# Optimization experiments

Measured on AMD Instinct MI355X. Metric: run time of the kernel, lower is better.

Reference implementation:

```python
import jax, jax.numpy as jnp
import numpy as np

N_NODES = 20000
IN_DIM = 256
HID = 128
N_CLASSES = 64
N_EDGES = 320000
EPS_BN = 1e-5


def setup_inputs() -> dict:
    key = jax.random.key(0)
    ks = jax.random.split(key, 24)
    s = 0.1
    inp = {}
    inp['x'] = jax.random.normal(ks[0], (N_NODES, IN_DIM), dtype=jnp.float32)
    inp['edge_index'] = jax.random.randint(ks[1], (2, N_EDGES), 0, N_NODES, dtype=jnp.int32)
    # GATConv 1: in=IN_DIM, out=HID per head, heads=4, concat=False
    inp['W1'] = s * jax.random.normal(ks[2], (IN_DIM, 4 * HID), dtype=jnp.float32)
    inp['a_src1'] = s * jax.random.normal(ks[3], (4, HID), dtype=jnp.float32)
    inp['a_dst1'] = s * jax.random.normal(ks[4], (4, HID), dtype=jnp.float32)
    inp['b1'] = jnp.zeros((HID,), jnp.float32)
    # GATConv 2: in=HID, out=HID per head, heads=4, concat=False
    inp['W2'] = s * jax.random.normal(ks[5], (HID, 4 * HID), dtype=jnp.float32)
    inp['a_src2'] = s * jax.random.normal(ks[6], (4, HID), dtype=jnp.float32)
    inp['a_dst2'] = s * jax.random.normal(ks[7], (4, HID), dtype=jnp.float32)
    inp['b2'] = jnp.zeros((HID,), jnp.float32)
    # GATConv 3: heads=1, concat=True (default)
    inp['W3'] = s * jax.random.normal(ks[8], (HID, HID), dtype=jnp.float32)
    inp['a_src3'] = s * jax.random.normal(ks[9], (1, HID), dtype=jnp.float32)
    inp['a_dst3'] = s * jax.random.normal(ks[10], (1, HID), dtype=jnp.float32)
    inp['b3'] = jnp.zeros((HID,), jnp.float32)
    # BatchNorm (eval-mode running stats)
    for i, k in zip((1, 2), (ks[11], ks[12])):
        inp[f'bn{i}_g'] = jnp.ones((HID,), jnp.float32)
        inp[f'bn{i}_b'] = jnp.zeros((HID,), jnp.float32)
        inp[f'bn{i}_m'] = 0.01 * jax.random.normal(k, (HID,), dtype=jnp.float32)
        inp[f'bn{i}_v'] = jnp.ones((HID,), jnp.float32)
    # classifier MLP
    inp['l1_w'] = s * jax.random.normal(ks[13], (HID, HID), dtype=jnp.float32)
    inp['l1_b'] = jnp.zeros((HID,), jnp.float32)
    inp['l2_w'] = s * jax.random.normal(ks[14], (HID, HID // 2), dtype=jnp.float32)
    inp['l2_b'] = jnp.zeros((HID // 2,), jnp.float32)
    inp['l3_w'] = s * jax.random.normal(ks[15], (HID // 2, N_CLASSES), dtype=jnp.float32)
    inp['l3_b'] = jnp.zeros((N_CLASSES,), jnp.float32)
    return inp


def _gat(x, src, dst, W, a_src, a_dst, b, heads, out_ch, concat):
    """PyG GATConv (with self-loops already appended to src/dst)."""
    n = x.shape[0]
    h = (x @ W).reshape(n, heads, out_ch)            # [N,H,C]
    alpha_s = jnp.sum(h * a_src[None], axis=-1)       # [N,H]
    alpha_d = jnp.sum(h * a_dst[None], axis=-1)       # [N,H]
    e = jax.nn.leaky_relu(alpha_s[src] + alpha_d[dst], 0.2)  # [E,H]
    # segment softmax over incoming edges of each destination node
    m = jax.ops.segment_max(e, dst, num_segments=n)
    m = jnp.where(jnp.isfinite(m), m, 0.0)
    ex = jnp.exp(e - m[dst])
    den = jax.ops.segment_sum(ex, dst, num_segments=n)
    alpha = ex / (den[dst] + 1e-16)                   # [E,H]
    msg = h[src] * alpha[:, :, None]                  # [E,H,C]
    out = jax.ops.segment_sum(msg, dst, num_segments=n)  # [N,H,C]
    out = out.reshape(n, heads * out_ch) if concat else out.mean(axis=1)
    return out + b


def _bn_eval(x, g, b, m, v):
    return g * (x - m) * jax.lax.rsqrt(v + EPS_BN) + b


def reference(x, edge_index, W1, a_src1, a_dst1, b1, W2, a_src2, a_dst2, b2,
              W3, a_src3, a_dst3, b3, bn1_g, bn1_b, bn1_m, bn1_v,
              bn2_g, bn2_b, bn2_m, bn2_v, l1_w, l1_b, l2_w, l2_b, l3_w, l3_b):
    n = x.shape[0]
    loops = jnp.arange(n, dtype=edge_index.dtype)
    src = jnp.concatenate([edge_index[0], loops])
    dst = jnp.concatenate([edge_index[1], loops])

    h = _gat(x, src, dst, W1, a_src1, a_dst1, b1, 4, HID, False)
    h = jax.nn.relu(_bn_eval(h, bn1_g, bn1_b, bn1_m, bn1_v))
    h = _gat(h, src, dst, W2, a_src2, a_dst2, b2, 4, HID, False)
    h = jax.nn.relu(_bn_eval(h, bn2_g, bn2_b, bn2_m, bn2_v))
    h = _gat(h, src, dst, W3, a_src3, a_dst3, b3, 1, HID, True)

    h = jax.nn.relu(h @ l1_w + l1_b)
    h = jax.nn.relu(h @ l2_w + l2_b)
    return jax.nn.sigmoid(h @ l3_w + l3_b)  # [N, num_labels]
```

## Files before the change

### kernel.cpp

```cpp
#include <hip/hip_runtime.h>
#include <cstdint>
#include <cstddef>

#define NN 20000

typedef __bf16 bf16_t;
typedef __bf16 bf16x8 __attribute__((ext_vector_type(8)));
typedef float f32x4 __attribute__((ext_vector_type(4)));

#define AS1 __attribute__((address_space(1)))
#define AS3 __attribute__((address_space(3)))

__device__ __forceinline__ float lrelu(float x) { return x >= 0.f ? x : 0.2f * x; }
__device__ __forceinline__ float bflo(uint32_t u) { return __uint_as_float(u << 16); }
__device__ __forceinline__ float bfhi(uint32_t u) { return __uint_as_float(u & 0xffff0000u); }

__device__ __forceinline__ uint32_t pack2bf(float a, float b) {
  bf16_t x = (bf16_t)a, y = (bf16_t)b;
  uint16_t ux = __builtin_bit_cast(uint16_t, x);
  uint16_t uy = __builtin_bit_cast(uint16_t, y);
  return (uint32_t)ux | ((uint32_t)uy << 16);
}


__global__ __launch_bounds__(1024) void scan_kernel(const int* __restrict__ cnt,
                                                    int* __restrict__ row_ptr,
                                                    int* __restrict__ cursor, int n) {
  __shared__ int wsum[16];
  const int t = threadIdx.x;
  const int lane = t & 63, w = t >> 6;
  int carry = 0;
  for (int base = 0; base < n; base += 1024) {
    int i = base + t;
    int v = (i < n) ? cnt[i] : 0;
    int x = v;
#pragma unroll
    for (int d = 1; d < 64; d <<= 1) {
      int y = __shfl_up(x, d);
      if (lane >= d) x += y;
    }
    if (lane == 63) wsum[w] = x;
    __syncthreads();
    if (t < 16) {
      int s = wsum[t];
#pragma unroll
      for (int d = 1; d < 16; d <<= 1) {
        int y = __shfl_up(s, d);
        if (t >= d) s += y;
      }
      wsum[t] = s;
    }
    __syncthreads();
    int blocksum = wsum[15];
    int wprefix = (w == 0) ? 0 : wsum[w - 1];
    int excl = carry + wprefix + (x - v);
    if (i < n) { row_ptr[i] = excl; cursor[i] = excl; }
    carry += blocksum;
    __syncthreads();
  }
  if (t == 0) row_ptr[n] = carry;
}


struct WDesc { const float* W; bf16_t* Bt; int K; int Cw; int H; float scale; int b0; };
struct WPack { WDesc d[4]; };

struct Prep1Args {
  WPack wp;
  const float *W1, *as1, *ad1, *W2, *as2, *ad2, *W3, *as3, *ad3;
  float *P1, *P2, *P3;
  const float *W3m, *L1w, *b3v, *l1b;
  bf16_t* M3t; float* bm;
  const int* ei; int E, N, EB;
  int* cnt;
};

__global__ __launch_bounds__(256) void prep1(Prep1Args a) {
  __shared__ float tile[32][33];
  const int b = blockIdx.x;
  const int t = threadIdx.x;

  if (b < 204) {
    int i = 3;
#pragma unroll
    for (int k = 2; k >= 0; --k)
      if (b < a.wp.d[k + 1].b0) i = k;
    const WDesc de = a.wp.d[i];
    const int bi = b - de.b0;
    const int ktiles = de.K / 32;
    const int kt = bi % ktiles, rt = bi / ktiles;
    const int gc = rt * 32;
    const int h = gc / de.Cw, c0 = gc % de.Cw;
    const int tx = t & 31, ty = t >> 5;
#pragma unroll
    for (int r = 0; r < 32; r += 8)
      tile[ty + r][tx] = de.W[(size_t)(kt * 32 + ty + r) * (de.H * de.Cw) + h * de.Cw + c0 + tx];
    __syncthreads();
#pragma unroll
    for (int r = 0; r < 32; r += 8)
      de.Bt[(size_t)(c0 + ty + r) * (de.H * de.K) + h * de.K + kt * 32 + tx] =
          (bf16_t)(de.scale * tile[tx][ty + r]);
  } else if (b < 716) {
    const int kk = b - 204;
    const float *W, *asrc, *adst;
    float* P;
    int K, H, k;
    if (kk < 256)      { W = a.W1; asrc = a.as1; adst = a.ad1; P = a.P1; K = 256; H = 4; k = kk; }
    else if (kk < 384) { W = a.W2; asrc = a.as2; adst = a.ad2; P = a.P2; K = 128; H = 4; k = kk - 256; }
    else               { W = a.W3; asrc = a.as3; adst = a.ad3; P = a.P3; K = 128; H = 1; k = kk - 384; }
    for (int j = 0; j < 2 * H; ++j) {
      const int h = (j < H) ? j : j - H;
      const float* av = (j < H) ? asrc : adst;
      float pv = 0.f;
      if (t < 128) pv = W[(size_t)k * (H * 128) + h * 128 + t] * av[h * 128 + t];
#pragma unroll
      for (int d = 1; d < 64; d <<= 1) pv += __shfl_xor(pv, d);
      if (t == 0 || t == 64) tile[0][t >> 6] = pv;
      __syncthreads();
      if (t == 0) P[j * K + k] = tile[0][0] + tile[0][1];
      __syncthreads();
    }
  } else if (b < 780) {
    const int idx = (b - 716) * 256 + t;
    const int k = idx >> 7, c = idx & 127;
    float s = 0.f;
    for (int m = 0; m < 128; ++m) s += a.W3m[k * 128 + m] * a.L1w[m * 128 + c];
    a.M3t[c * 128 + k] = (bf16_t)s;
    if (k == 0) {
      float tt = a.l1b[c];
      for (int m = 0; m < 128; ++m) tt += a.b3v[m] * a.L1w[m * 128 + c];
      a.bm[c] = tt;
    }
  } else {
    const int i = (b - 780) * 256 + t;
    if (i < a.E + a.N) {
      int dst = (i < a.E) ? a.ei[a.E + i] : (i - a.E);
      atomicAdd(&a.cnt[dst], 1);
    }
  }
}


__global__ __launch_bounds__(256) void scatter_cast(const int* __restrict__ ei, int E, int N,
                                                    int EB, int* __restrict__ cursor,
                                                    int* __restrict__ col,
                                                    const float* __restrict__ x,
                                                    const float* __restrict__ P1,
                                                    bf16_t* __restrict__ xb,
                                                    float* __restrict__ asadA) {
  const int b = blockIdx.x, t = threadIdx.x;
  if (b < EB) {
    const int i = b * 256 + t;
    if (i < E + N) {
      int src, dst;
      if (i < E) { src = ei[i]; dst = ei[E + i]; }
      else       { src = i - E; dst = src; }
      int slot = atomicAdd(&cursor[dst], 1);
      col[slot] = src;
    }
  } else {
    const int wv = t >> 6, lane = t & 63;
    const int n = (b - EB) * 4 + wv;
    const float4 v = *(const float4*)&x[(size_t)n * 256 + lane * 4];
    uint2 ov;
    ov.x = pack2bf(v.x, v.y);
    ov.y = pack2bf(v.z, v.w);
    *(uint2*)&xb[(size_t)n * 256 + lane * 4] = ov;
    float s[8];
#pragma unroll
    for (int j = 0; j < 8; ++j) {
      const float4 pj = *(const float4*)&P1[j * 256 + lane * 4];
      s[j] = v.x * pj.x + v.y * pj.y + v.z * pj.z + v.w * pj.w;
    }
#pragma unroll
    for (int j = 0; j < 8; ++j)
#pragma unroll
      for (int d = 1; d < 64; d <<= 1) s[j] += __shfl_xor(s[j], d);
    if (lane == 0) {
#pragma unroll
      for (int j = 0; j < 8; ++j) asadA[(size_t)n * 8 + j] = s[j];
    }
  }
}


template <int TN, int ACT, typename OUT_T>
__global__ __launch_bounds__(256) void gemm_mfma(const bf16_t* __restrict__ A,
                                                 const bf16_t* __restrict__ Bt,
                                                 const float* __restrict__ bias,
                                                 const float* __restrict__ bng,
                                                 const float* __restrict__ bnb,
                                                 const float* __restrict__ bnm,
                                                 const float* __restrict__ bnv,
                                                 OUT_T* __restrict__ C,
                                                 int M, int N, int K) {
  constexpr int TM = 128, BK = 64;
  constexpr int MT = (TN == 128) ? 4 : 2;
  constexpr int NRB = (TN * BK * 2) / 4096;
  __shared__ __align__(16) bf16_t As[TM * BK];
  __shared__ __align__(16) bf16_t Bs[TN * BK];

  const int t = threadIdx.x;
  const int wave = t >> 6, lane = t & 63;
  const int ln15 = lane & 15, quad = lane >> 4;
  const int bm = blockIdx.x * TM;
  const int bn = blockIdx.y * TN;
  const int wm = (TN == 128) ? (wave >> 1) * 64 : wave * 32;
  const int wn = (TN == 128) ? (wave & 1) * 64 : 0;
  const int rowLimA = M - 1 - bm;
  const size_t strideAB = (size_t)K * 2;

  f32x4 acc[MT][4];
#pragma unroll
  for (int mi = 0; mi < MT; ++mi)
#pragma unroll
    for (int ni = 0; ni < 4; ++ni) acc[mi][ni] = (f32x4){0.f, 0.f, 0.f, 0.f};

  const char* gA = (const char*)(A + (size_t)bm * K);
  const char* gB = (const char*)(Bt + (size_t)bn * K);

  for (int k0 = 0; k0 < K; k0 += BK) {
#pragma unroll
    for (int r = 0; r < 4; ++r) {
      int base = (wave * 4 + r) * 1024;
      int flat = base + lane * 16;
      int row = flat >> 7;
      int grow = row < rowLimA ? row : rowLimA;
      const char* gp = gA + (size_t)grow * strideAB + (size_t)(k0 * 2) + (flat & 127);
      __builtin_amdgcn_global_load_lds((const AS1 void*)gp,
                                       (AS3 void*)((char*)As + base), 16, 0, 0);
    }
#pragma unroll
    for (int r = 0; r < NRB; ++r) {
      int base = (wave * NRB + r) * 1024;
      int flat = base + lane * 16;
      int row = flat >> 7;
      const char* gp = gB + (size_t)row * strideAB + (size_t)(k0 * 2) + (flat & 127);
      __builtin_amdgcn_global_load_lds((const AS1 void*)gp,
                                       (AS3 void*)((char*)Bs + base), 16, 0, 0);
    }
    __syncthreads();
#pragma unroll
    for (int kk = 0; kk < BK; kk += 32) {
      bf16x8 af[MT], bfr[4];
#pragma unroll
      for (int mi = 0; mi < MT; ++mi)
        af[mi] = *(const bf16x8*)&As[(wm + mi * 16 + ln15) * BK + kk + quad * 8];
#pragma unroll
      for (int ni = 0; ni < 4; ++ni)
        bfr[ni] = *(const bf16x8*)&Bs[(wn + ni * 16 + ln15) * BK + kk + quad * 8];
#pragma unroll
      for (int mi = 0; mi < MT; ++mi)
#pragma unroll
        for (int ni = 0; ni < 4; ++ni)
          acc[mi][ni] = __builtin_amdgcn_mfma_f32_16x16x32_bf16(af[mi], bfr[ni], acc[mi][ni], 0, 0, 0);
    }
    __syncthreads();
  }

#pragma unroll
  for (int mi = 0; mi < MT; ++mi) {
    int r0 = bm + wm + mi * 16 + quad * 4;
#pragma unroll
    for (int ni = 0; ni < 4; ++ni) {
      int c = bn + wn + ni * 16 + ln15;
      float bv = bias ? bias[c] : 0.f;
      float sc = 1.f, sh = 0.f;
      if (ACT == 3) {
        sc = bng[c] * rsqrtf(bnv[c] + 1e-5f);
        sh = bnb[c] - bnm[c] * sc;
      }
#pragma unroll
      for (int reg = 0; reg < 4; ++reg) {
        int r = r0 + reg;
        if (r < M) {
          float v = acc[mi][ni][reg] + bv;
          if (ACT == 1) v = fmaxf(v, 0.f);
          else if (ACT == 3) v = fmaxf(v * sc + sh, 0.f);
          C[(size_t)r * N + c] = (OUT_T)v;
        }
      }
    }
  }
}


template <int K, int H>
__global__ __launch_bounds__(256) void alpha_gemm(const bf16_t* __restrict__ f,
                                                  const float* __restrict__ P,
                                                  float* __restrict__ asad) {
  constexpr int J = 2 * H;
  constexpr int KC = K / 64;
  const int wv = threadIdx.x >> 6, lane = threadIdx.x & 63;
  const int n = blockIdx.x * 4 + wv;
  float v[KC];
  if (KC == 4) {
    uint2 pv = *(const uint2*)&f[(size_t)n * K + lane * 4];
    v[0] = bflo(pv.x); v[1] = bfhi(pv.x); v[2] = bflo(pv.y); v[3] = bfhi(pv.y);
  } else {
    uint32_t pv = *(const uint32_t*)&f[(size_t)n * K + lane * 2];
    v[0] = bflo(pv); v[1] = bfhi(pv);
  }
  float s[J];
#pragma unroll
  for (int j = 0; j < J; ++j) {
    float acc = 0.f;
#pragma unroll
    for (int q = 0; q < KC; ++q) acc += v[q] * P[j * K + lane * KC + q];
    s[j] = acc;
  }
#pragma unroll
  for (int j = 0; j < J; ++j)
#pragma unroll
    for (int d = 1; d < 64; d <<= 1) s[j] += __shfl_xor(s[j], d);
  if (lane == 0) {
#pragma unroll
    for (int j = 0; j < J; ++j) asad[(size_t)n * J + j] = s[j];
  }
}


template <int K>
__global__ __launch_bounds__(128) void gat_agg_in4(const bf16_t* __restrict__ f,
                                                   const float* __restrict__ asad,
                                                   const int* __restrict__ rp,
                                                   const int* __restrict__ cs,
                                                   bf16_t* __restrict__ agg) {
  constexpr int KC = K / 64;
  const int wv = threadIdx.x >> 6, lane = threadIdx.x & 63;
  const int n = blockIdx.x * 2 + wv;
  __shared__ int sb[2][64];
  __shared__ float4 wl[2][64];

  const int r0 = rp[n], r1 = rp[n + 1];
  const int deg = r1 - r0;
  const float4 adv = *(const float4*)&asad[(size_t)n * 8 + 4];
  const char* fb = (const char*)f;
  const size_t loff = (size_t)lane * (KC * 2);

  float acc[4][KC];
#pragma unroll
  for (int j = 0; j < 4; ++j)
#pragma unroll
    for (int q = 0; q < KC; ++q) acc[j][q] = 0.f;

  auto edge_fma = [&](const char* gp, float4 w4) {
    if (KC == 4) {
      uint2 b = *(const uint2*)gp;
      float v0 = bflo(b.x), v1 = bfhi(b.x), v2 = bflo(b.y), v3 = bfhi(b.y);
      acc[0][0] += w4.x * v0; acc[0][1] += w4.x * v1; acc[0][2] += w4.x * v2; acc[0][3] += w4.x * v3;
      acc[1][0] += w4.y * v0; acc[1][1] += w4.y * v1; acc[1][2] += w4.y * v2; acc[1][3] += w4.y * v3;
      acc[2][0] += w4.z * v0; acc[2][1] += w4.z * v1; acc[2][2] += w4.z * v2; acc[2][3] += w4.z * v3;
      acc[3][0] += w4.w * v0; acc[3][1] += w4.w * v1; acc[3][2] += w4.w * v2; acc[3][3] += w4.w * v3;
    } else {
      uint32_t b = *(const uint32_t*)gp;
      float v0 = bflo(b), v1 = bfhi(b);
      acc[0][0] += w4.x * v0; acc[0][1] += w4.x * v1;
      acc[1][0] += w4.y * v0; acc[1][1] += w4.y * v1;
      acc[2][0] += w4.z * v0; acc[2][1] += w4.z * v1;
      acc[3][0] += w4.w * v0; acc[3][1] += w4.w * v1;
    }
  };

  if (deg <= 64) {
    const bool valid = lane < deg;
    int s = 0;
    float e0 = -1e30f, e1 = -1e30f, e2 = -1e30f, e3 = -1e30f;
    if (valid) {
      s = cs[r0 + lane];
      const float4 av = *(const float4*)&asad[(size_t)s * 8];
      e0 = lrelu(av.x + adv.x); e1 = lrelu(av.y + adv.y);
      e2 = lrelu(av.z + adv.z); e3 = lrelu(av.w + adv.w);
    }
    float m0 = e0, m1 = e1, m2 = e2, m3 = e3;
#pragma unroll
    for (int d = 1; d < 64; d <<= 1) {
      m0 = fmaxf(m0, __shfl_xor(m0, d)); m1 = fmaxf(m1, __shfl_xor(m1, d));
      m2 = fmaxf(m2, __shfl_xor(m2, d)); m3 = fmaxf(m3, __shfl_xor(m3, d));
    }
    float x0 = valid ? __expf(e0 - m0) : 0.f;
    float x1 = valid ? __expf(e1 - m1) : 0.f;
    float x2 = valid ? __expf(e2 - m2) : 0.f;
    float x3 = valid ? __expf(e3 - m3) : 0.f;
    float d0 = x0, d1 = x1, d2 = x2, d3 = x3;
#pragma unroll
    for (int d = 1; d < 64; d <<= 1) {
      d0 += __shfl_xor(d0, d); d1 += __shfl_xor(d1, d);
      d2 += __shfl_xor(d2, d); d3 += __shfl_xor(d3, d);
    }
    if (valid) {
      sb[wv][lane] = s * (K * 2);
      wl[wv][lane] = make_float4(x0 / (d0 + 1e-16f), x1 / (d1 + 1e-16f),
                                 x2 / (d2 + 1e-16f), x3 / (d3 + 1e-16f));
    }
    __builtin_amdgcn_wave_barrier();

    int g = 0;
    for (; g + 8 <= deg; g += 8) {
      const char* p[8];
      float4 w[8];
#pragma unroll
      for (int k = 0; k < 8; ++k) { p[k] = fb + (size_t)sb[wv][g + k] + loff; w[k] = wl[wv][g + k]; }
      if (KC == 4) {
        uint2 b[8];
#pragma unroll
        for (int k = 0; k < 8; ++k) b[k] = *(const uint2*)p[k];
#pragma unroll
        for (int k = 0; k < 8; ++k) {
          float v0 = bflo(b[k].x), v1 = bfhi(b[k].x), v2 = bflo(b[k].y), v3 = bfhi(b[k].y);
          acc[0][0] += w[k].x * v0; acc[0][1] += w[k].x * v1; acc[0][2] += w[k].x * v2; acc[0][3] += w[k].x * v3;
          acc[1][0] += w[k].y * v0; acc[1][1] += w[k].y * v1; acc[1][2] += w[k].y * v2; acc[1][3] += w[k].y * v3;
          acc[2][0] += w[k].z * v0; acc[2][1] += w[k].z * v1; acc[2][2] += w[k].z * v2; acc[2][3] += w[k].z * v3;
          acc[3][0] += w[k].w * v0; acc[3][1] += w[k].w * v1; acc[3][2] += w[k].w * v2; acc[3][3] += w[k].w * v3;
        }
      } else {
        uint32_t b[8];
#pragma unroll
        for (int k = 0; k < 8; ++k) b[k] = *(const uint32_t*)p[k];
#pragma unroll
        for (int k = 0; k < 8; ++k) {
          float v0 = bflo(b[k]), v1 = bfhi(b[k]);
          acc[0][0] += w[k].x * v0; acc[0][1] += w[k].x * v1;
          acc[1][0] += w[k].y * v0; acc[1][1] += w[k].y * v1;
          acc[2][0] += w[k].z * v0; acc[2][1] += w[k].z * v1;
          acc[3][0] += w[k].w * v0; acc[3][1] += w[k].w * v1;
        }
      }
    }
    for (; g < deg; ++g)
      edge_fma(fb + (size_t)sb[wv][g] + loff, wl[wv][g]);
  } else {
    float m0 = -1e30f, m1 = -1e30f, m2 = -1e30f, m3 = -1e30f;
    for (int i = r0 + lane; i < r1; i += 64) {
      const float4 av = *(const float4*)&asad[(size_t)cs[i] * 8];
      m0 = fmaxf(m0, lrelu(av.x + adv.x)); m1 = fmaxf(m1, lrelu(av.y + adv.y));
      m2 = fmaxf(m2, lrelu(av.z + adv.z)); m3 = fmaxf(m3, lrelu(av.w + adv.w));
    }
#pragma unroll
    for (int d = 1; d < 64; d <<= 1) {
      m0 = fmaxf(m0, __shfl_xor(m0, d)); m1 = fmaxf(m1, __shfl_xor(m1, d));
      m2 = fmaxf(m2, __shfl_xor(m2, d)); m3 = fmaxf(m3, __shfl_xor(m3, d));
    }
    float d0 = 0.f, d1 = 0.f, d2 = 0.f, d3 = 0.f;
    for (int i = r0 + lane; i < r1; i += 64) {
      const float4 av = *(const float4*)&asad[(size_t)cs[i] * 8];
      d0 += __expf(lrelu(av.x + adv.x) - m0); d1 += __expf(lrelu(av.y + adv.y) - m1);
      d2 += __expf(lrelu(av.z + adv.z) - m2); d3 += __expf(lrelu(av.w + adv.w) - m3);
    }
#pragma unroll
    for (int d = 1; d < 64; d <<= 1) {
      d0 += __shfl_xor(d0, d); d1 += __shfl_xor(d1, d);
      d2 += __shfl_xor(d2, d); d3 += __shfl_xor(d3, d);
    }
    const float i0 = 1.f / (d0 + 1e-16f), i1 = 1.f / (d1 + 1e-16f);
    const float i2 = 1.f / (d2 + 1e-16f), i3 = 1.f / (d3 + 1e-16f);
    for (int base = r0; base < r1; base += 64) {
      const int ne = min(64, r1 - base);
      if (lane < ne) {
        const int s = cs[base + lane];
        const float4 av = *(const float4*)&asad[(size_t)s * 8];
        sb[wv][lane] = s * (K * 2);
        wl[wv][lane] = make_float4(__expf(lrelu(av.x + adv.x) - m0) * i0,
                                   __expf(lrelu(av.y + adv.y) - m1) * i1,
                                   __expf(lrelu(av.z + adv.z) - m2) * i2,
                                   __expf(lrelu(av.w + adv.w) - m3) * i3);
      }
      __builtin_amdgcn_wave_barrier();
      for (int g = 0; g < ne; ++g)
        edge_fma(fb + (size_t)sb[wv][g] + loff, wl[wv][g]);
      __builtin_amdgcn_wave_barrier();
    }
  }

#pragma unroll
  for (int j = 0; j < 4; ++j) {
    if (KC == 4) {
      uint2 ov;
      ov.x = pack2bf(acc[j][0], acc[j][1]);
      ov.y = pack2bf(acc[j][2], acc[j][3]);
      *(uint2*)&agg[(size_t)n * (4 * K) + j * K + lane * 4] = ov;
    } else {
      *(uint32_t*)&agg[(size_t)n * (4 * K) + j * K + lane * 2] = pack2bf(acc[j][0], acc[j][1]);
    }
  }
}


__global__ __launch_bounds__(128) void gat_agg_in1(const bf16_t* __restrict__ f,
                                                   const float* __restrict__ asad,
                                                   const int* __restrict__ rp,
                                                   const int* __restrict__ cs,
                                                   bf16_t* __restrict__ agg) {
  const int wv = threadIdx.x >> 6, lane = threadIdx.x & 63;
  const int n = blockIdx.x * 2 + wv;
  __shared__ int sb[2][64];
  __shared__ float wl[2][64];

  const int r0 = rp[n], r1 = rp[n + 1];
  const int deg = r1 - r0;
  const float adv = asad[(size_t)n * 2 + 1];
  const char* fb = (const char*)f;
  const size_t loff = (size_t)lane * 4;
  float a0 = 0.f, a1 = 0.f;

  auto fma2 = [&](uint32_t v, float w) { a0 += w * bflo(v); a1 += w * bfhi(v); };

  if (deg <= 64) {
    const bool valid = lane < deg;
    int s = 0;
    float e = -1e30f;
    if (valid) { s = cs[r0 + lane]; e = lrelu(asad[(size_t)s * 2] + adv); }
    float m = e;
#pragma unroll
    for (int d = 1; d < 64; d <<= 1) m = fmaxf(m, __shfl_xor(m, d));
    float x = valid ? __expf(e - m) : 0.f;
    float den = x;
#pragma unroll
    for (int d = 1; d < 64; d <<= 1) den += __shfl_xor(den, d);
    if (valid) { sb[wv][lane] = s * 256; wl[wv][lane] = x / (den + 1e-16f); }
    __builtin_amdgcn_wave_barrier();
    int g = 0;
    for (; g + 8 <= deg; g += 8) {
      uint32_t b[8];
      float w[8];
#pragma unroll
      for (int k = 0; k < 8; ++k) {
        b[k] = *(const uint32_t*)(fb + (size_t)sb[wv][g + k] + loff);
        w[k] = wl[wv][g + k];
      }
#pragma unroll
      for (int k = 0; k < 8; ++k) { a0 += w[k] * bflo(b[k]); a1 += w[k] * bfhi(b[k]); }
    }
    for (; g < deg; ++g)
      fma2(*(const uint32_t*)(fb + (size_t)sb[wv][g] + loff), wl[wv][g]);
  } else {
    float m = -1e30f;
    for (int i = r0 + lane; i < r1; i += 64) m = fmaxf(m, lrelu(asad[(size_t)cs[i] * 2] + adv));
#pragma unroll
    for (int d = 1; d < 64; d <<= 1) m = fmaxf(m, __shfl_xor(m, d));
    float den = 0.f;
    for (int i = r0 + lane; i < r1; i += 64) den += __expf(lrelu(asad[(size_t)cs[i] * 2] + adv) - m);
#pragma unroll
    for (int d = 1; d < 64; d <<= 1) den += __shfl_xor(den, d);
    const float dinv = 1.f / (den + 1e-16f);
    for (int base = r0; base < r1; base += 64) {
      const int ne = min(64, r1 - base);
      if (lane < ne) {
        const int s = cs[base + lane];
        sb[wv][lane] = s * 256;
        wl[wv][lane] = __expf(lrelu(asad[(size_t)s * 2] + adv) - m) * dinv;
      }
      __builtin_amdgcn_wave_barrier();
      for (int g = 0; g < ne; ++g)
        fma2(*(const uint32_t*)(fb + (size_t)sb[wv][g] + loff), wl[wv][g]);
      __builtin_amdgcn_wave_barrier();
    }
  }
  *(uint32_t*)&agg[(size_t)n * 128 + lane * 2] = pack2bf(a0, a1);
}


__global__ __launch_bounds__(256) void mlp_tail(const bf16_t* __restrict__ A,
                                                const bf16_t* __restrict__ M3t,
                                                const float* __restrict__ bm,
                                                const bf16_t* __restrict__ l2t,
                                                const float* __restrict__ l2b,
                                                const bf16_t* __restrict__ l3t,
                                                const float* __restrict__ l3b,
                                                float* __restrict__ out, int M) {
  __shared__ __align__(16) bf16_t As[128 * 128];
  __shared__ __align__(16) bf16_t Ws[128 * 128];
  const int t = threadIdx.x, wave = t >> 6, lane = t & 63;
  const int ln15 = lane & 15, quad = lane >> 4;
  const int bmr = blockIdx.x * 128;
  const int rowLim = M - 1 - bmr;

#pragma unroll
  for (int r = 0; r < 8; ++r) {
    int base = (wave * 8 + r) * 1024;
    int flat = base + lane * 16;
    int row = flat >> 8;
    int grow = row < rowLim ? row : rowLim;
    const char* gp = (const char*)A + (size_t)grow * 256 + (flat & 255);
    __builtin_amdgcn_global_load_lds((const AS1 void*)gp,
                                     (AS3 void*)((char*)As + base), 16, 0, 0);
  }
#pragma unroll
  for (int r = 0; r < 8; ++r) {
    int base = (wave * 8 + r) * 1024;
    __builtin_amdgcn_global_load_lds((const AS1 void*)((const char*)M3t + base + lane * 16),
                                     (AS3 void*)((char*)Ws + base), 16, 0, 0);
  }
  __syncthreads();

  const int wm = wave * 32;
  f32x4 a1[2][8];
#pragma unroll
  for (int mi = 0; mi < 2; ++mi)
#pragma unroll
    for (int ni = 0; ni < 8; ++ni) a1[mi][ni] = (f32x4){0.f, 0.f, 0.f, 0.f};
#pragma unroll
  for (int kk = 0; kk < 128; kk += 32) {
    bf16x8 af[2];
#pragma unroll
    for (int mi = 0; mi < 2; ++mi)
      af[mi] = *(const bf16x8*)&As[(wm + mi * 16 + ln15) * 128 + kk + quad * 8];
#pragma unroll
    for (int ni = 0; ni < 8; ++ni) {
      bf16x8 bf = *(const bf16x8*)&Ws[(ni * 16 + ln15) * 128 + kk + quad * 8];
#pragma unroll
      for (int mi = 0; mi < 2; ++mi)
        a1[mi][ni] = __builtin_amdgcn_mfma_f32_16x16x32_bf16(af[mi], bf, a1[mi][ni], 0, 0, 0);
    }
  }
  __syncthreads();

#pragma unroll
  for (int r = 0; r < 4; ++r) {
    int base = (wave * 4 + r) * 1024;
    __builtin_amdgcn_global_load_lds((const AS1 void*)((const char*)l2t + base + lane * 16),
                                     (AS3 void*)((char*)Ws + base), 16, 0, 0);
  }
#pragma unroll
  for (int r = 0; r < 2; ++r) {
    int base = (wave * 2 + r) * 1024;
    __builtin_amdgcn_global_load_lds((const AS1 void*)((const char*)l3t + base + lane * 16),
                                     (AS3 void*)((char*)Ws + 8192 * 2 + base), 16, 0, 0);
  }
#pragma unroll
  for (int mi = 0; mi < 2; ++mi) {
    int r0 = wm + mi * 16 + quad * 4;
#pragma unroll
    for (int ni = 0; ni < 8; ++ni) {
      int c = ni * 16 + ln15;
      float bv = bm[c];
#pragma unroll
      for (int reg = 0; reg < 4; ++reg)
        As[(r0 + reg) * 128 + c] = (bf16_t)fmaxf(a1[mi][ni][reg] + bv, 0.f);
    }
  }
  __syncthreads();

  f32x4 a2[2][4];
#pragma unroll
  for (int mi = 0; mi < 2; ++mi)
#pragma unroll
    for (int ni = 0; ni < 4; ++ni) a2[mi][ni] = (f32x4){0.f, 0.f, 0.f, 0.f};
#pragma unroll
  for (int kk = 0; kk < 128; kk += 32) {
    bf16x8 af[2];
#pragma unroll
    for (int mi = 0; mi < 2; ++mi)
      af[mi] = *(const bf16x8*)&As[(wm + mi * 16 + ln15) * 128 + kk + quad * 8];
#pragma unroll
    for (int ni = 0; ni < 4; ++ni) {
      bf16x8 bf = *(const bf16x8*)&Ws[(ni * 16 + ln15) * 128 + kk + quad * 8];
#pragma unroll
      for (int mi = 0; mi < 2; ++mi)
        a2[mi][ni] = __builtin_amdgcn_mfma_f32_16x16x32_bf16(af[mi], bf, a2[mi][ni], 0, 0, 0);
    }
  }
  __syncthreads();

#pragma unroll
  for (int mi = 0; mi < 2; ++mi) {
    int r0 = wm + mi * 16 + quad * 4;
#pragma unroll
    for (int ni = 0; ni < 4; ++ni) {
      int c = ni * 16 + ln15;
      float bv = l2b[c];
#pragma unroll
      for (int reg = 0; reg < 4; ++reg)
        As[(r0 + reg) * 64 + c] = (bf16_t)fmaxf(a2[mi][ni][reg] + bv, 0.f);
    }
  }
  __syncthreads();

  f32x4 a3[2][4];
#pragma unroll
  for (int mi = 0; mi < 2; ++mi)
#pragma unroll
    for (int ni = 0; ni < 4; ++ni) a3[mi][ni] = (f32x4){0.f, 0.f, 0.f, 0.f};
#pragma unroll
  for (int kk = 0; kk < 64; kk += 32) {
    bf16x8 af[2];
#pragma unroll
    for (int mi = 0; mi < 2; ++mi)
      af[mi] = *(const bf16x8*)&As[(wm + mi * 16 + ln15) * 64 + kk + quad * 8];
#pragma unroll
    for (int ni = 0; ni < 4; ++ni) {
      bf16x8 bf = *(const bf16x8*)&Ws[8192 + (ni * 16 + ln15) * 64 + kk + quad * 8];
#pragma unroll
      for (int mi = 0; mi < 2; ++mi)
        a3[mi][ni] = __builtin_amdgcn_mfma_f32_16x16x32_bf16(af[mi], bf, a3[mi][ni], 0, 0, 0);
    }
  }
#pragma unroll
  for (int mi = 0; mi < 2; ++mi) {
    int r0 = wm + mi * 16 + quad * 4;
#pragma unroll
    for (int ni = 0; ni < 4; ++ni) {
      int c = ni * 16 + ln15;
      float bv = l3b[c];
#pragma unroll
      for (int reg = 0; reg < 4; ++reg) {
        int r = bmr + r0 + reg;
        if (r < M) {
          float v = a3[mi][ni][reg] + bv;
          out[(size_t)r * 64 + c] = 1.f / (1.f + __expf(-v));
        }
      }
    }
  }
}


extern "C" void kernel_launch(void* const* d_in, const int* in_sizes, int n_in,
                              void* d_out, int out_size, void* d_ws, size_t ws_size,
                              hipStream_t stream) {
  const float* x      = (const float*)d_in[0];
  const int*   ei     = (const int*)d_in[1];
  const float* W1     = (const float*)d_in[2];
  const float* a_src1 = (const float*)d_in[3];
  const float* a_dst1 = (const float*)d_in[4];
  const float* b1     = (const float*)d_in[5];
  const float* W2     = (const float*)d_in[6];
  const float* a_src2 = (const float*)d_in[7];
  const float* a_dst2 = (const float*)d_in[8];
  const float* b2     = (const float*)d_in[9];
  const float* W3     = (const float*)d_in[10];
  const float* a_src3 = (const float*)d_in[11];
  const float* a_dst3 = (const float*)d_in[12];
  const float* b3     = (const float*)d_in[13];
  const float* bn1g = (const float*)d_in[14];
  const float* bn1b = (const float*)d_in[15];
  const float* bn1m = (const float*)d_in[16];
  const float* bn1v = (const float*)d_in[17];
  const float* bn2g = (const float*)d_in[18];
  const float* bn2b = (const float*)d_in[19];
  const float* bn2m = (const float*)d_in[20];
  const float* bn2v = (const float*)d_in[21];
  const float* l1w = (const float*)d_in[22];
  const float* l1b = (const float*)d_in[23];
  const float* l2w = (const float*)d_in[24];
  const float* l2b = (const float*)d_in[25];
  const float* l3w = (const float*)d_in[26];
  const float* l3b = (const float*)d_in[27];
  float* out = (float*)d_out;

  const int N = NN;
  const int E = in_sizes[1] / 2;
  const int ET = E + N;
  const int EB = (ET + 255) / 256;

  char* p = (char*)d_ws;
  auto carve = [&](size_t bytes) {
    char* q = p;
    p += (bytes + 255) & ~(size_t)255;
    return q;
  };
  bf16_t* xb    = (bf16_t*)carve((size_t)N * 256 * 2);
  bf16_t* aggb  = (bf16_t*)carve((size_t)N * 1024 * 2);
  bf16_t* f1b   = (bf16_t*)carve((size_t)N * 128 * 2);
  bf16_t* f2b   = (bf16_t*)carve((size_t)N * 128 * 2);
  float* asadA  = (float*)carve((size_t)N * 8 * 4);
  float* asadB  = (float*)carve((size_t)N * 8 * 4);
  float* asadC  = (float*)carve((size_t)N * 2 * 4);
  int* cnt      = (int*)carve((size_t)N * 4);
  int* cursor   = (int*)carve((size_t)N * 4);
  int* row_ptr  = (int*)carve((size_t)(N + 1) * 4);
  int* col      = (int*)carve((size_t)ET * 4);
  bf16_t* Ws1t  = (bf16_t*)carve((size_t)128 * 1024 * 2);
  bf16_t* Ws2t  = (bf16_t*)carve((size_t)128 * 512 * 2);
  bf16_t* M3t   = (bf16_t*)carve((size_t)128 * 128 * 2);
  bf16_t* l2t   = (bf16_t*)carve((size_t)64 * 128 * 2);
  bf16_t* l3t   = (bf16_t*)carve((size_t)64 * 64 * 2);
  float* P1     = (float*)carve((size_t)8 * 256 * 4);
  float* P2     = (float*)carve((size_t)8 * 128 * 4);
  float* P3     = (float*)carve((size_t)2 * 128 * 4);
  float* bm     = (float*)carve((size_t)128 * 4);
  (void)ws_size; (void)n_in; (void)out_size;

  hipMemsetAsync(cnt, 0, (size_t)N * 4, stream);

  Prep1Args pa;
  pa.wp.d[0] = {W1,  Ws1t, 256, 128, 4, 0.25f, 0};
  pa.wp.d[1] = {W2,  Ws2t, 128, 128, 4, 0.25f, 128};
  pa.wp.d[2] = {l2w, l2t,  128, 64,  1, 1.0f,  192};
  pa.wp.d[3] = {l3w, l3t,  64,  64,  1, 1.0f,  200};
  pa.W1 = W1; pa.as1 = a_src1; pa.ad1 = a_dst1;
  pa.W2 = W2; pa.as2 = a_src2; pa.ad2 = a_dst2;
  pa.W3 = W3; pa.as3 = a_src3; pa.ad3 = a_dst3;
  pa.P1 = P1; pa.P2 = P2; pa.P3 = P3;
  pa.W3m = W3; pa.L1w = l1w; pa.b3v = b3; pa.l1b = l1b;
  pa.M3t = M3t; pa.bm = bm;
  pa.ei = ei; pa.E = E; pa.N = N; pa.EB = EB;
  pa.cnt = cnt;
  prep1<<<780 + EB, 256, 0, stream>>>(pa);

  scan_kernel<<<1, 1024, 0, stream>>>(cnt, row_ptr, cursor, N);
  scatter_cast<<<EB + N / 4, 256, 0, stream>>>(ei, E, N, EB, cursor, col, x, P1, xb, asadA);

  const int gm = (N + 127) / 128;
  const int ab = N / 4;
  const int gb = N / 2;

  gat_agg_in4<256><<<gb, 128, 0, stream>>>(xb, asadA, row_ptr, col, aggb);
  gemm_mfma<64, 3, bf16_t><<<dim3(gm, 2), 256, 0, stream>>>(
      aggb, Ws1t, b1, bn1g, bn1b, bn1m, bn1v, f1b, N, 128, 1024);

  alpha_gemm<128, 4><<<ab, 256, 0, stream>>>(f1b, P2, asadB);
  gat_agg_in4<128><<<gb, 128, 0, stream>>>(f1b, asadB, row_ptr, col, aggb);
  gemm_mfma<64, 3, bf16_t><<<dim3(gm, 2), 256, 0, stream>>>(
      aggb, Ws2t, b2, bn2g, bn2b, bn2m, bn2v, f2b, N, 128, 512);

  alpha_gemm<128, 1><<<ab, 256, 0, stream>>>(f2b, P3, asadC);
  gat_agg_in1<<<gb, 128, 0, stream>>>(f2b, asadC, row_ptr, col, aggb);
  mlp_tail<<<gm, 256, 0, stream>>>(aggb, M3t, bm, l2t, l2b, l3t, l3b, out, N);
}
```

Measured before the change: 337.9 us.

## Fuse post-scan pipeline into one persistent cooperative kernel with grid syncs

Replaces the sequence of separate launches (scatter/cast, three gathers, two GEMMs, two alpha projections, MLP tail) with one cooperative persistent kernel. Stages are separated by grid-wide barriers, and blocks loop over tiles or node groups in grid-stride fashion. The fused MLP tail is split into three separate GEMM stages that round-trip through global memory, and the aggregation now packs four nodes per block instead of two. This removes launch gaps and tail effects, but adds grid.sync costs, lower occupancy for the gather stages, and extra global traffic in the MLP.

```diff
diff --git a/kernel.cpp b/kernel.cpp
--- a/kernel.cpp
+++ b/kernel.cpp
@@ -1,6 +1,9 @@
 #include <hip/hip_runtime.h>
+#include <hip/hip_cooperative_groups.h>
 #include <cstdint>
 #include <cstddef>
+
+namespace cg = cooperative_groups;
 
 #define NN 20000
 
@@ -141,35 +144,46 @@
 }
 
 
-__global__ __launch_bounds__(256) void scatter_cast(const int* __restrict__ ei, int E, int N,
-                                                    int EB, int* __restrict__ cursor,
-                                                    int* __restrict__ col,
-                                                    const float* __restrict__ x,
-                                                    const float* __restrict__ P1,
-                                                    bf16_t* __restrict__ xb,
-                                                    float* __restrict__ asadA) {
-  const int b = blockIdx.x, t = threadIdx.x;
-  if (b < EB) {
+struct MegaArgs {
+  const int* ei; int E, N, EB;
+  int* cursor; int* col;
+  const float* x; const float* P1;
+  bf16_t* xb; float* asadA;
+  bf16_t *aggb, *f1b, *f2b;
+  float *asadB, *asadC;
+  const int* rp;
+  const bf16_t *Ws1t, *Ws2t, *M3t, *l2t, *l3t;
+  const float *P2, *P3;
+  const float *b1, *bn1g, *bn1b, *bn1m, *bn1v;
+  const float *b2, *bn2g, *bn2b, *bn2m, *bn2v;
+  const float *bm, *l2b, *l3b;
+  float* out;
+};
+
+
+__device__ void scatter_cast_dev(const MegaArgs& a, int b) {
+  const int t = threadIdx.x;
+  if (b < a.EB) {
     const int i = b * 256 + t;
-    if (i < E + N) {
+    if (i < a.E + a.N) {
       int src, dst;
-      if (i < E) { src = ei[i]; dst = ei[E + i]; }
-      else       { src = i - E; dst = src; }
-      int slot = atomicAdd(&cursor[dst], 1);
-      col[slot] = src;
+      if (i < a.E) { src = a.ei[i]; dst = a.ei[a.E + i]; }
+      else         { src = i - a.E; dst = src; }
+      int slot = atomicAdd(&a.cursor[dst], 1);
+      a.col[slot] = src;
     }
   } else {
     const int wv = t >> 6, lane = t & 63;
-    const int n = (b - EB) * 4 + wv;
-    const float4 v = *(const float4*)&x[(size_t)n * 256 + lane * 4];
+    const int n = (b - a.EB) * 4 + wv;
+    const float4 v = *(const float4*)&a.x[(size_t)n * 256 + lane * 4];
     uint2 ov;
     ov.x = pack2bf(v.x, v.y);
     ov.y = pack2bf(v.z, v.w);
-    *(uint2*)&xb[(size_t)n * 256 + lane * 4] = ov;
+    *(uint2*)&a.xb[(size_t)n * 256 + lane * 4] = ov;
     float s[8];
 #pragma unroll
     for (int j = 0; j < 8; ++j) {
-      const float4 pj = *(const float4*)&P1[j * 256 + lane * 4];
+      const float4 pj = *(const float4*)&a.P1[j * 256 + lane * 4];
       s[j] = v.x * pj.x + v.y * pj.y + v.z * pj.z + v.w * pj.w;
     }
 #pragma unroll
@@ -178,540 +192,422 @@
       for (int d = 1; d < 64; d <<= 1) s[j] += __shfl_xor(s[j], d);
     if (lane == 0) {
 #pragma unroll
-      for (int j = 0; j < 8; ++j) asadA[(size_t)n * 8 + j] = s[j];
+      for (int j = 0; j < 8; ++j) a.asadA[(size_t)n * 8 + j] = s[j];
     }
   }
 }
 
-
-template <int TN, int ACT, typename OUT_T>
-__global__ __launch_bounds__(256) void gemm_mfma(const bf16_t* __restrict__ A,
-                                                 const bf16_t* __restrict__ Bt,
-                                                 const float* __restrict__ bias,
-                                                 const float* __restrict__ bng,
-                                                 const float* __restrict__ bnb,
-                                                 const float* __restrict__ bnm,
-                                                 const float* __restrict__ bnv,
-                                                 OUT_T* __restrict__ C,
-                                                 int M, int N, int K) {
-  constexpr int TM = 128, BK = 64;
-  constexpr int MT = (TN == 128) ? 4 : 2;
-  constexpr int NRB = (TN * BK * 2) / 4096;
-  __shared__ __align__(16) bf16_t As[TM * BK];
-  __shared__ __align__(16) bf16_t Bs[TN * BK];
-
+__device__ void gemm_dev(char* smem, const bf16_t* A, const bf16_t* Bt,
+                         const float* bias, const float* bng, const float* bnb,
+                         const float* bnm, const float* bnv, int act,
+                         bf16_t* Cb, float* Cf, int M, int N, int K) {
+  bf16_t* As = (bf16_t*)smem;
+  bf16_t* Bs = (bf16_t*)(smem + 16384);
   const int t = threadIdx.x;
   const int wave = t >> 6, lane = t & 63;
   const int ln15 = lane & 15, quad = lane >> 4;
-  const int bm = blockIdx.x * TM;
-  const int bn = blockIdx.y * TN;
-  const int wm = (TN == 128) ? (wave >> 1) * 64 : wave * 32;
-  const int wn = (TN == 128) ? (wave & 1) * 64 : 0;
-  const int rowLimA = M - 1 - bm;
+  const int gx = (M + 127) >> 7;
+  const int ntile = gx * (N >> 6);
   const size_t strideAB = (size_t)K * 2;
 
-  f32x4 acc[MT][4];
-#pragma unroll
-  for (int mi = 0; mi < MT; ++mi)
-#pragma unroll
-    for (int ni = 0; ni < 4; ++ni) acc[mi][ni] = (f32x4){0.f, 0.f, 0.f, 0.f};
-
-  const char* gA = (const char*)(A + (size_t)bm * K);
-  const char* gB = (const char*)(Bt + (size_t)bn * K);
-
-  for (int k0 = 0; k0 < K; k0 += BK) {
-#pragma unroll
-    for (int r = 0; r < 4; ++r) {
-      int base = (wave * 4 + r) * 1024;
-      int flat = base + lane * 16;
-      int row = flat >> 7;
-      int grow = row < rowLimA ? row : rowLimA;
-      const char* gp = gA + (size_t)grow * strideAB + (size_t)(k0 * 2) + (flat & 127);
-      __builtin_amdgcn_global_load_lds((const AS1 void*)gp,
-                                       (AS3 void*)((char*)As + base), 16, 0, 0);
-    }
-#pragma unroll
-    for (int r = 0; r < NRB; ++r) {
-      int base = (wave * NRB + r) * 1024;
-      int flat = base + lane * 16;
-      int row = flat >> 7;
-      const char* gp = gB + (size_t)row * strideAB + (size_t)(k0 * 2) + (flat & 127);
-      __builtin_amdgcn_global_load_lds((const AS1 void*)gp,
-                                       (AS3 void*)((char*)Bs + base), 16, 0, 0);
-    }
-    __syncthreads();
-#pragma unroll
-    for (int kk = 0; kk < BK; kk += 32) {
-      bf16x8 af[MT], bfr[4];
-#pragma unroll
-      for (int mi = 0; mi < MT; ++mi)
-        af[mi] = *(const bf16x8*)&As[(wm + mi * 16 + ln15) * BK + kk + quad * 8];
-#pragma unroll
-      for (int ni = 0; ni < 4; ++ni)
-        bfr[ni] = *(const bf16x8*)&Bs[(wn + ni * 16 + ln15) * BK + kk + quad * 8];
-#pragma unroll
-      for (int mi = 0; mi < MT; ++mi)
+  for (int tile = blockIdx.x; tile < ntile; tile += gridDim.x) {
+    const int bm = (tile % gx) * 128;
+    const int bn = (tile / gx) * 64;
+    const int wm = wave * 32;
+    const int rowLimA = M - 1 - bm;
+
+    f32x4 acc[2][4];
+#pragma unroll
+    for (int mi = 0; mi < 2; ++mi)
+#pragma unroll
+      for (int ni = 0; ni < 4; ++ni) acc[mi][ni] = (f32x4){0.f, 0.f, 0.f, 0.f};
+
+    const char* gA = (const char*)A + (size_t)bm * strideAB;
+    const char* gB = (const char*)Bt + (size_t)bn * strideAB;
+
+    for (int k0 = 0; k0 < K; k0 += 64) {
+#pragma unroll
+      for (int r = 0; r < 4; ++r) {
+        int base = (wave * 4 + r) * 1024;
+        int flat = base + lane * 16;
+        int row = flat >> 7;
+        int grow = row < rowLimA ? row : rowLimA;
+        const char* gp = gA + (size_t)grow * strideAB + (size_t)(k0 * 2) + (flat & 127);
+        __builtin_amdgcn_global_load_lds((const AS1 void*)gp,
+                                         (AS3 void*)((char*)As + base), 16, 0, 0);
+      }
+#pragma unroll
+      for (int r = 0; r < 2; ++r) {
+        int base = (wave * 2 + r) * 1024;
+        int flat = base + lane * 16;
+        int row = flat >> 7;
+        const char* gp = gB + (size_t)row * strideAB + (size_t)(k0 * 2) + (flat & 127);
+        __builtin_amdgcn_global_load_lds((const AS1 void*)gp,
+                                         (AS3 void*)((char*)Bs + base), 16, 0, 0);
+      }
+      __syncthreads();
+#pragma unroll
+      for (int kk = 0; kk < 64; kk += 32) {
+        bf16x8 af[2], bfr[4];
+#pragma unroll
+        for (int mi = 0; mi < 2; ++mi)
+          af[mi] = *(const bf16x8*)&As[(wm + mi * 16 + ln15) * 64 + kk + quad * 8];
 #pragma unroll
         for (int ni = 0; ni < 4; ++ni)
-          acc[mi][ni] = __builtin_amdgcn_mfma_f32_16x16x32_bf16(af[mi], bfr[ni], acc[mi][ni], 0, 0, 0);
-    }
-    __syncthreads();
+          bfr[ni] = *(const bf16x8*)&Bs[(ni * 16 + ln15) * 64 + kk + quad * 8];
+#pragma unroll
+        for (int mi = 0; mi < 2; ++mi)
+#pragma unroll
+          for (int ni = 0; ni < 4; ++ni)
+            acc[mi][ni] = __builtin_amdgcn_mfma_f32_16x16x32_bf16(af[mi], bfr[ni], acc[mi][ni], 0, 0, 0);
+      }
+      __syncthreads();
+    }
+
+#pragma unroll
+    for (int mi = 0; mi < 2; ++mi) {
+      int r0 = bm + wm + mi * 16 + quad * 4;
+#pragma unroll
+      for (int ni = 0; ni < 4; ++ni) {
+        int c = bn + ni * 16 + ln15;
+        float bv = bias[c];
+        float sc = 1.f, sh = 0.f;
+        if (act == 3) {
+          sc = bng[c] * rsqrtf(bnv[c] + 1e-5f);
+          sh = bnb[c] - bnm[c] * sc;
+        }
+#pragma unroll
+        for (int reg = 0; reg < 4; ++reg) {
+          int r = r0 + reg;
+          if (r < M) {
+            float v = acc[mi][ni][reg] + bv;
+            if (act == 1) v = fmaxf(v, 0.f);
+            else if (act == 2) v = 1.f / (1.f + __expf(-v));
+            else v = fmaxf(v * sc + sh, 0.f);
+            if (Cb) Cb[(size_t)r * N + c] = (bf16_t)v;
+            else    Cf[(size_t)r * N + c] = v;
+          }
+        }
+      }
+    }
   }
-
-#pragma unroll
-  for (int mi = 0; mi < MT; ++mi) {
-    int r0 = bm + wm + mi * 16 + quad * 4;
-#pragma unroll
-    for (int ni = 0; ni < 4; ++ni) {
-      int c = bn + wn + ni * 16 + ln15;
-      float bv = bias ? bias[c] : 0.f;
-      float sc = 1.f, sh = 0.f;
-      if (ACT == 3) {
-        sc = bng[c] * rsqrtf(bnv[c] + 1e-5f);
-        sh = bnb[c] - bnm[c] * sc;
-      }
-#pragma unroll
-      for (int reg = 0; reg < 4; ++reg) {
-        int r = r0 + reg;
-        if (r < M) {
-          float v = acc[mi][ni][reg] + bv;
-          if (ACT == 1) v = fmaxf(v, 0.f);
-          else if (ACT == 3) v = fmaxf(v * sc + sh, 0.f);
-          C[(size_t)r * N + c] = (OUT_T)v;
-        }
-      }
-    }
-  }
-}
-
+}
 
 template <int K, int H>
-__global__ __launch_bounds__(256) void alpha_gemm(const bf16_t* __restrict__ f,
-                                                  const float* __restrict__ P,
-                                                  float* __restrict__ asad) {
+__device__ void alpha_dev(const bf16_t* f, const float* P, float* asad, int N) {
   constexpr int J = 2 * H;
   constexpr int KC = K / 64;
   const int wv = threadIdx.x >> 6, lane = threadIdx.x & 63;
-  const int n = blockIdx.x * 4 + wv;
-  float v[KC];
-  if (KC == 4) {
-    uint2 pv = *(const uint2*)&f[(size_t)n * K + lane * 4];
-    v[0] = bflo(pv.x); v[1] = bfhi(pv.x); v[2] = bflo(pv.y); v[3] = bfhi(pv.y);
-  } else {
-    uint32_t pv = *(const uint32_t*)&f[(size_t)n * K + lane * 2];
-    v[0] = bflo(pv); v[1] = bfhi(pv);
+  for (int grp = blockIdx.x; grp < N / 4; grp += gridDim.x) {
+    const int n = grp * 4 + wv;
+    float v[KC];
+    if (KC == 4) {
+      uint2 pv = *(const uint2*)&f[(size_t)n * K + lane * 4];
+      v[0] = bflo(pv.x); v[1] = bfhi(pv.x); v[2] = bflo(pv.y); v[3] = bfhi(pv.y);
+    } else {
+      uint32_t pv = *(const uint32_t*)&f[(size_t)n * K + lane * 2];
+      v[0] = bflo(pv); v[1] = bfhi(pv);
+    }
+    float s[J];
+#pragma unroll
+    for (int j = 0; j < J; ++j) {
+      float acc = 0.f;
+#pragma unroll
+      for (int q = 0; q < KC; ++q) acc += v[q] * P[j * K + lane * KC + q];
+      s[j] = acc;
+    }
+#pragma unroll
+    for (int j = 0; j < J; ++j)
+#pragma unroll
+      for (int d = 1; d < 64; d <<= 1) s[j] += __shfl_xor(s[j], d);
+    if (lane == 0) {
+#pragma unroll
+      for (int j = 0; j < J; ++j) asad[(size_t)n * J + j] = s[j];
+    }
   }
-  float s[J];
-#pragma unroll
-  for (int j = 0; j < J; ++j) {
-    float acc = 0.f;
-#pragma unroll
-    for (int q = 0; q < KC; ++q) acc += v[q] * P[j * K + lane * KC + q];
-    s[j] = acc;
-  }
-#pragma unroll
-  for (int j = 0; j < J; ++j)
-#pragma unroll
-    for (int d = 1; d < 64; d <<= 1) s[j] += __shfl_xor(s[j], d);
-  if (lane == 0) {
-#pragma unroll
-    for (int j = 0; j < J; ++j) asad[(size_t)n * J + j] = s[j];
-  }
-}
-
+}
 
 template <int K>
-__global__ __launch_bounds__(128) void gat_agg_in4(const bf16_t* __restrict__ f,
-                                                   const float* __restrict__ asad,
-                                                   const int* __restrict__ rp,
-                                                   const int* __restrict__ cs,
-                                                   bf16_t* __restrict__ agg) {
+__device__ void gather4_dev(char* smem, const bf16_t* f, const float* asad,
+                            const int* rp, const int* cs, bf16_t* agg, int N) {
   constexpr int KC = K / 64;
+  int* sb = (int*)smem;
+  float4* wl = (float4*)(smem + 1024);
   const int wv = threadIdx.x >> 6, lane = threadIdx.x & 63;
-  const int n = blockIdx.x * 2 + wv;
-  __shared__ int sb[2][64];
-  __shared__ float4 wl[2][64];
-
-  const int r0 = rp[n], r1 = rp[n + 1];
-  const int deg = r1 - r0;
-  const float4 adv = *(const float4*)&asad[(size_t)n * 8 + 4];
   const char* fb = (const char*)f;
   const size_t loff = (size_t)lane * (KC * 2);
 
-  float acc[4][KC];
-#pragma unroll
-  for (int j = 0; j < 4; ++j)
-#pragma unroll
-    for (int q = 0; q < KC; ++q) acc[j][q] = 0.f;
-
-  auto edge_fma = [&](const char* gp, float4 w4) {
-    if (KC == 4) {
-      uint2 b = *(const uint2*)gp;
-      float v0 = bflo(b.x), v1 = bfhi(b.x), v2 = bflo(b.y), v3 = bfhi(b.y);
-      acc[0][0] += w4.x * v0; acc[0][1] += w4.x * v1; acc[0][2] += w4.x * v2; acc[0][3] += w4.x * v3;
-      acc[1][0] += w4.y * v0; acc[1][1] += w4.y * v1; acc[1][2] += w4.y * v2; acc[1][3] += w4.y * v3;
-      acc[2][0] += w4.z * v0; acc[2][1] += w4.z * v1; acc[2][2] += w4.z * v2; acc[2][3] += w4.z * v3;
-      acc[3][0] += w4.w * v0; acc[3][1] += w4.w * v1; acc[3][2] += w4.w * v2; acc[3][3] += w4.w * v3;
+  for (int grp = blockIdx.x; grp < N / 4; grp += gridDim.x) {
+    const int n = grp * 4 + wv;
+    const int r0 = rp[n], r1 = rp[n + 1];
+    const int deg = r1 - r0;
+    const float4 adv = *(const float4*)&asad[(size_t)n * 8 + 4];
+
+    float acc[4][KC];
+#pragma unroll
+    for (int j = 0; j < 4; ++j)
+#pragma unroll
+      for (int q = 0; q < KC; ++q) acc[j][q] = 0.f;
+
+    auto edge_fma = [&](const char* gp, float4 w4) {
+      if (KC == 4) {
+        uint2 b = *(const uint2*)gp;
+        float v0 = bflo(b.x), v1 = bfhi(b.x), v2 = bflo(b.y), v3 = bfhi(b.y);
+        acc[0][0] += w4.x * v0; acc[0][1] += w4.x * v1; acc[0][2] += w4.x * v2; acc[0][3] += w4.x * v3;
+        acc[1][0] += w4.y * v0; acc[1][1] += w4.y * v1; acc[1][2] += w4.y * v2; acc[1][3] += w4.y * v3;
+        acc[2][0] += w4.z * v0; acc[2][1] += w4.z * v1; acc[2][2] += w4.z * v2; acc[2][3] += w4.z * v3;
+        acc[3][0] += w4.w * v0; acc[3][1] += w4.w * v1; acc[3][2] += w4.w * v2; acc[3][3] += w4.w * v3;
+      } else {
+        uint32_t b = *(const uint32_t*)gp;
+        float v0 = bflo(b), v1 = bfhi(b);
+        acc[0][0] += w4.x * v0; acc[0][1] += w4.x * v1;
+        acc[1][0] += w4.y * v0; acc[1][1] += w4.y * v1;
+        acc[2][0] += w4.z * v0; acc[2][1] += w4.z * v1;
+        acc[3][0] += w4.w * v0; acc[3][1] += w4.w * v1;
+      }
+    };
+
+    if (deg <= 64) {
+      const bool valid = lane < deg;
+      int s = 0;
+      float e0 = -1e30f, e1 = -1e30f, e2 = -1e30f, e3 = -1e30f;
+      if (valid) {
+        s = cs[r0 + lane];
+        const float4 av = *(const float4*)&asad[(size_t)s * 8];
+        e0 = lrelu(av.x + adv.x); e1 = lrelu(av.y + adv.y);
+        e2 = lrelu(av.z + adv.z); e3 = lrelu(av.w + adv.w);
+      }
+      float m0 = e0, m1 = e1, m2 = e2, m3 = e3;
+#pragma unroll
+      for (int d = 1; d < 64; d <<= 1) {
+        m0 = fmaxf(m0, __shfl_xor(m0, d)); m1 = fmaxf(m1, __shfl_xor(m1, d));
+        m2 = fmaxf(m2, __shfl_xor(m2, d)); m3 = fmaxf(m3, __shfl_xor(m3, d));
+      }
+      float x0 = valid ? __expf(e0 - m0) : 0.f;
+      float x1 = valid ? __expf(e1 - m1) : 0.f;
+      float x2 = valid ? __expf(e2 - m2) : 0.f;
+      float x3 = valid ? __expf(e3 - m3) : 0.f;
+      float d0 = x0, d1 = x1, d2 = x2, d3 = x3;
+#pragma unroll
+      for (int d = 1; d < 64; d <<= 1) {
+        d0 += __shfl_xor(d0, d); d1 += __shfl_xor(d1, d);
+        d2 += __shfl_xor(d2, d); d3 += __shfl_xor(d3, d);
+      }
+      if (valid) {
+        sb[wv * 64 + lane] = s * (K * 2);
+        wl[wv * 64 + lane] = make_float4(x0 / (d0 + 1e-16f), x1 / (d1 + 1e-16f),
+                                         x2 / (d2 + 1e-16f), x3 / (d3 + 1e-16f));
+      }
+      __builtin_amdgcn_wave_barrier();
+
+      int g = 0;
+      for (; g + 8 <= deg; g += 8) {
+        const char* p[8];
+        float4 w[8];
+#pragma unroll
+        for (int k = 0; k < 8; ++k) {
+          p[k] = fb + (size_t)sb[wv * 64 + g + k] + loff;
+          w[k] = wl[wv * 64 + g + k];
+        }
+        if (KC == 4) {
+          uint2 b[8];
+#pragma unroll
+          for (int k = 0; k < 8; ++k) b[k] = *(const uint2*)p[k];
+#pragma unroll
+          for (int k = 0; k < 8; ++k) {
+            float v0 = bflo(b[k].x), v1 = bfhi(b[k].x), v2 = bflo(b[k].y), v3 = bfhi(b[k].y);
+            acc[0][0] += w[k].x * v0; acc[0][1] += w[k].x * v1; acc[0][2] += w[k].x * v2; acc[0][3] += w[k].x * v3;
+            acc[1][0] += w[k].y * v0; acc[1][1] += w[k].y * v1; acc[1][2] += w[k].y * v2; acc[1][3] += w[k].y * v3;
+            acc[2][0] += w[k].z * v0; acc[2][1] += w[k].z * v1; acc[2][2] += w[k].z * v2; acc[2][3] += w[k].z * v3;
+            acc[3][0] += w[k].w * v0; acc[3][1] += w[k].w * v1; acc[3][2] += w[k].w * v2; acc[3][3] += w[k].w * v3;
+          }
+        } else {
+          uint32_t b[8];
+#pragma unroll
+          for (int k = 0; k < 8; ++k) b[k] = *(const uint32_t*)p[k];
+#pragma unroll
+          for (int k = 0; k < 8; ++k) {
+            float v0 = bflo(b[k]), v1 = bfhi(b[k]);
+            acc[0][0] += w[k].x * v0; acc[0][1] += w[k].x * v1;
+            acc[1][0] += w[k].y * v0; acc[1][1] += w[k].y * v1;
+            acc[2][0] += w[k].z * v0; acc[2][1] += w[k].z * v1;
+            acc[3][0] += w[k].w * v0; acc[3][1] += w[k].w * v1;
+          }
+        }
+      }
+      for (; g < deg; ++g)
+        edge_fma(fb + (size_t)sb[wv * 64 + g] + loff, wl[wv * 64 + g]);
     } else {
-      uint32_t b = *(const uint32_t*)gp;
-      float v0 = bflo(b), v1 = bfhi(b);
-      acc[0][0] += w4.x * v0; acc[0][1] += w4.x * v1;
-      acc[1][0] += w4.y * v0; acc[1][1] += w4.y * v1;
-      acc[2][0] += w4.z * v0; acc[2][1] += w4.z * v1;
-      acc[3][0] += w4.w * v0; acc[3][1] += w4.w * v1;
-    }
-  };
-
-  if (deg <= 64) {
-    const bool valid = lane < deg;
-    int s = 0;
-    float e0 = -1e30f, e1 = -1e30f, e2 = -1e30f, e3 = -1e30f;
-    if (valid) {
-      s = cs[r0 + lane];
-      const float4 av = *(const float4*)&asad[(size_t)s * 8];
-      e0 = lrelu(av.x + adv.x); e1 = lrelu(av.y + adv.y);
-      e2 = lrelu(av.z + adv.z); e3 = lrelu(av.w + adv.w);
-    }
-    float m0 = e0, m1 = e1, m2 = e2, m3 = e3;
-#pragma unroll
-    for (int d = 1; d < 64; d <<= 1) {
-      m0 = fmaxf(m0, __shfl_xor(m0, d)); m1 = fmaxf(m1, __shfl_xor(m1, d));
-      m2 = fmaxf(m2, __shfl_xor(m2, d)); m3 = fmaxf(m3, __shfl_xor(m3, d));
-    }
-    float x0 = valid ? __expf(e0 - m0) : 0.f;
-    float x1 = valid ? __expf(e1 - m1) : 0.f;
-    float x2 = valid ? __expf(e2 - m2) : 0.f;
-    float x3 = valid ? __expf(e3 - m3) : 0.f;
-    float d0 = x0, d1 = x1, d2 = x2, d3 = x3;
-#pragma unroll
-    for (int d = 1; d < 64; d <<= 1) {
-      d0 += __shfl_xor(d0, d); d1 += __shfl_xor(d1, d);
-      d2 += __shfl_xor(d2, d); d3 += __shfl_xor(d3, d);
-    }
-    if (valid) {
-      sb[wv][lane] = s * (K * 2);
-      wl[wv][lane] = make_float4(x0 / (d0 + 1e-16f), x1 / (d1 + 1e-16f),
-                                 x2 / (d2 + 1e-16f), x3 / (d3 + 1e-16f));
-    }
-    __builtin_amdgcn_wave_barrier();
-
-    int g = 0;
-    for (; g + 8 <= deg; g += 8) {
-      const char* p[8];
-      float4 w[8];
-#pragma unroll
-      for (int k = 0; k < 8; ++k) { p[k] = fb + (size_t)sb[wv][g + k] + loff; w[k] = wl[wv][g + k]; }
+      float m0 = -1e30f, m1 = -1e30f, m2 = -1e30f, m3 = -1e30f;
+      for (int i = r0 + lane; i < r1; i += 64) {
+        const float4 av = *(const float4*)&asad[(size_t)cs[i] * 8];
+        m0 = fmaxf(m0, lrelu(av.x + adv.x)); m1 = fmaxf(m1, lrelu(av.y + adv.y));
+        m2 = fmaxf(m2, lrelu(av.z + adv.z)); m3 = fmaxf(m3, lrelu(av.w + adv.w));
+      }
+#pragma unroll
+      for (int d = 1; d < 64; d <<= 1) {
+        m0 = fmaxf(m0, __shfl_xor(m0, d)); m1 = fmaxf(m1, __shfl_xor(m1, d));
+        m2 = fmaxf(m2, __shfl_xor(m2, d)); m3 = fmaxf(m3, __shfl_xor(m3, d));
+      }
+      float d0 = 0.f, d1 = 0.f, d2 = 0.f, d3 = 0.f;
+      for (int i = r0 + lane; i < r1; i += 64) {
+        const float4 av = *(const float4*)&asad[(size_t)cs[i] * 8];
+        d0 += __expf(lrelu(av.x + adv.x) - m0); d1 += __expf(lrelu(av.y + adv.y) - m1);
+        d2 += __expf(lrelu(av.z + adv.z) - m2); d3 += __expf(lrelu(av.w + adv.w) - m3);
+      }
+#pragma unroll
+      for (int d = 1; d < 64; d <<= 1) {
+        d0 += __shfl_xor(d0, d); d1 += __shfl_xor(d1, d);
+        d2 += __shfl_xor(d2, d); d3 += __shfl_xor(d3, d);
+      }
+      const float i0 = 1.f / (d0 + 1e-16f), i1 = 1.f / (d1 + 1e-16f);
+      const float i2 = 1.f / (d2 + 1e-16f), i3 = 1.f / (d3 + 1e-16f);
+      for (int base = r0; base < r1; base += 64) {
+        const int ne = min(64, r1 - base);
+        if (lane < ne) {
+          const int s = cs[base + lane];
+          const float4 av = *(const float4*)&asad[(size_t)s * 8];
+          sb[wv * 64 + lane] = s * (K * 2);
+          wl[wv * 64 + lane] = make_float4(__expf(lrelu(av.x + adv.x) - m0) * i0,
+                                           __expf(lrelu(av.y + adv.y) - m1) * i1,
+                                           __expf(lrelu(av.z + adv.z) - m2) * i2,
+                                           __expf(lrelu(av.w + adv.w) - m3) * i3);
+        }
+        __builtin_amdgcn_wave_barrier();
+        for (int g = 0; g < ne; ++g)
+          edge_fma(fb + (size_t)sb[wv * 64 + g] + loff, wl[wv * 64 + g]);
+        __builtin_amdgcn_wave_barrier();
+      }
+    }
+
+#pragma unroll
+    for (int j = 0; j < 4; ++j) {
       if (KC == 4) {
-        uint2 b[8];
-#pragma unroll
-        for (int k = 0; k < 8; ++k) b[k] = *(const uint2*)p[k];
-#pragma unroll
-        for (int k = 0; k < 8; ++k) {
-          float v0 = bflo(b[k].x), v1 = bfhi(b[k].x), v2 = bflo(b[k].y), v3 = bfhi(b[k].y);
-          acc[0][0] += w[k].x * v0; acc[0][1] += w[k].x * v1; acc[0][2] += w[k].x * v2; acc[0][3] += w[k].x * v3;
-          acc[1][0] += w[k].y * v0; acc[1][1] += w[k].y * v1; acc[1][2] += w[k].y * v2; acc[1][3] += w[k].y * v3;
-          acc[2][0] += w[k].z * v0; acc[2][1] += w[k].z * v1; acc[2][2] += w[k].z * v2; acc[2][3] += w[k].z * v3;
-          acc[3][0] += w[k].w * v0; acc[3][1] += w[k].w * v1; acc[3][2] += w[k].w * v2; acc[3][3] += w[k].w * v3;
-        }
+        uint2 ov;
+        ov.x = pack2bf(acc[j][0], acc[j][1]);
+        ov.y = pack2bf(acc[j][2], acc[j][3]);
+        *(uint2*)&agg[(size_t)n * (4 * K) + j * K + lane * 4] = ov;
       } else {
-        uint32_t b[8];
-#pragma unroll
-        for (int k = 0; k < 8; ++k) b[k] = *(const uint32_t*)p[k];
-#pragma unroll
-        for (int k = 0; k < 8; ++k) {
-          float v0 = bflo(b[k]), v1 = bfhi(b[k]);
-          acc[0][0] += w[k].x * v0; acc[0][1] += w[k].x * v1;
-          acc[1][0] += w[k].y * v0; acc[1][1] += w[k].y * v1;
-          acc[2][0] += w[k].z * v0; acc[2][1] += w[k].z * v1;
-          acc[3][0] += w[k].w * v0; acc[3][1] += w[k].w * v1;
-        }
-      }
-    }
-    for (; g < deg; ++g)
-      edge_fma(fb + (size_t)sb[wv][g] + loff, wl[wv][g]);
-  } else {
-    float m0 = -1e30f, m1 = -1e30f, m2 = -1e30f, m3 = -1e30f;
-    for (int i = r0 + lane; i < r1; i += 64) {
-      const float4 av = *(const float4*)&asad[(size_t)cs[i] * 8];
-      m0 = fmaxf(m0, lrelu(av.x + adv.x)); m1 = fmaxf(m1, lrelu(av.y + adv.y));
-      m2 = fmaxf(m2, lrelu(av.z + adv.z)); m3 = fmaxf(m3, lrelu(av.w + adv.w));
-    }
-#pragma unroll
-    for (int d = 1; d < 64; d <<= 1) {
-      m0 = fmaxf(m0, __shfl_xor(m0, d)); m1 = fmaxf(m1, __shfl_xor(m1, d));
-      m2 = fmaxf(m2, __shfl_xor(m2, d)); m3 = fmaxf(m3, __shfl_xor(m3, d));
-    }
-    float d0 = 0.f, d1 = 0.f, d2 = 0.f, d3 = 0.f;
-    for (int i = r0 + lane; i < r1; i += 64) {
-      const float4 av = *(const float4*)&asad[(size_t)cs[i] * 8];
-      d0 += __expf(lrelu(av.x + adv.x) - m0); d1 += __expf(lrelu(av.y + adv.y) - m1);
-      d2 += __expf(lrelu(av.z + adv.z) - m2); d3 += __expf(lrelu(av.w + adv.w) - m3);
-    }
-#pragma unroll
-    for (int d = 1; d < 64; d <<= 1) {
-      d0 += __shfl_xor(d0, d); d1 += __shfl_xor(d1, d);
-      d2 += __shfl_xor(d2, d); d3 += __shfl_xor(d3, d);
-    }
-    const float i0 = 1.f / (d0 + 1e-16f), i1 = 1.f / (d1 + 1e-16f);
-    const float i2 = 1.f / (d2 + 1e-16f), i3 = 1.f / (d3 + 1e-16f);
-    for (int base = r0; base < r1; base += 64) {
-      const int ne = min(64, r1 - base);
-      if (lane < ne) {
-        const int s = cs[base + lane];
-        const float4 av = *(const float4*)&asad[(size_t)s * 8];
-        sb[wv][lane] = s * (K * 2);
-        wl[wv][lane] = make_float4(__expf(lrelu(av.x + adv.x) - m0) * i0,
-                                   __expf(lrelu(av.y + adv.y) - m1) * i1,
-                                   __expf(lrelu(av.z + adv.z) - m2) * i2,
-                                   __expf(lrelu(av.w + adv.w) - m3) * i3);
-      }
-      __builtin_amdgcn_wave_barrier();
-      for (int g = 0; g < ne; ++g)
-        edge_fma(fb + (size_t)sb[wv][g] + loff, wl[wv][g]);
-      __builtin_amdgcn_wave_barrier();
+        *(uint32_t*)&agg[(size_t)n * (4 * K) + j * K + lane * 2] = pack2bf(acc[j][0], acc[j][1]);
+      }
     }
   }
-
-#pragma unroll
-  for (int j = 0; j < 4; ++j) {
-    if (KC == 4) {
-      uint2 ov;
-      ov.x = pack2bf(acc[j][0], acc[j][1]);
-      ov.y = pack2bf(acc[j][2], acc[j][3]);
-      *(uint2*)&agg[(size_t)n * (4 * K) + j * K + lane * 4] = ov;
-    } else {
-      *(uint32_t*)&agg[(size_t)n * (4 * K) + j * K + lane * 2] = pack2bf(acc[j][0], acc[j][1]);
-    }
-  }
-}
-
-
-__global__ __launch_bounds__(128) void gat_agg_in1(const bf16_t* __restrict__ f,
-                                                   const float* __restrict__ asad,
-                                                   const int* __restrict__ rp,
-                                                   const int* __restrict__ cs,
-                                                   bf16_t* __restrict__ agg) {
+}
+
+__device__ void gather1_dev(char* smem, const bf16_t* f, const float* asad,
+                            const int* rp, const int* cs, bf16_t* agg, int N) {
+  int* sb = (int*)smem;
+  float* wl = (float*)(smem + 1024);
   const int wv = threadIdx.x >> 6, lane = threadIdx.x & 63;
-  const int n = blockIdx.x * 2 + wv;
-  __shared__ int sb[2][64];
-  __shared__ float wl[2][64];
-
-  const int r0 = rp[n], r1 = rp[n + 1];
-  const int deg = r1 - r0;
-  const float adv = asad[(size_t)n * 2 + 1];
   const char* fb = (const char*)f;
   const size_t loff = (size_t)lane * 4;
-  float a0 = 0.f, a1 = 0.f;
-
-  auto fma2 = [&](uint32_t v, float w) { a0 += w * bflo(v); a1 += w * bfhi(v); };
-
-  if (deg <= 64) {
-    const bool valid = lane < deg;
-    int s = 0;
-    float e = -1e30f;
-    if (valid) { s = cs[r0 + lane]; e = lrelu(asad[(size_t)s * 2] + adv); }
-    float m = e;
-#pragma unroll
-    for (int d = 1; d < 64; d <<= 1) m = fmaxf(m, __shfl_xor(m, d));
-    float x = valid ? __expf(e - m) : 0.f;
-    float den = x;
-#pragma unroll
-    for (int d = 1; d < 64; d <<= 1) den += __shfl_xor(den, d);
-    if (valid) { sb[wv][lane] = s * 256; wl[wv][lane] = x / (den + 1e-16f); }
-    __builtin_amdgcn_wave_barrier();
-    int g = 0;
-    for (; g + 8 <= deg; g += 8) {
-      uint32_t b[8];
-      float w[8];
-#pragma unroll
-      for (int k = 0; k < 8; ++k) {
-        b[k] = *(const uint32_t*)(fb + (size_t)sb[wv][g + k] + loff);
-        w[k] = wl[wv][g + k];
-      }
-#pragma unroll
-      for (int k = 0; k < 8; ++k) { a0 += w[k] * bflo(b[k]); a1 += w[k] * bfhi(b[k]); }
-    }
-    for (; g < deg; ++g)
-      fma2(*(const uint32_t*)(fb + (size_t)sb[wv][g] + loff), wl[wv][g]);
-  } else {
-    float m = -1e30f;
-    for (int i = r0 + lane; i < r1; i += 64) m = fmaxf(m, lrelu(asad[(size_t)cs[i] * 2] + adv));
-#pragma unroll
-    for (int d = 1; d < 64; d <<= 1) m = fmaxf(m, __shfl_xor(m, d));
-    float den = 0.f;
-    for (int i = r0 + lane; i < r1; i += 64) den += __expf(lrelu(asad[(size_t)cs[i] * 2] + adv) - m);
-#pragma unroll
-    for (int d = 1; d < 64; d <<= 1) den += __shfl_xor(den, d);
-    const float dinv = 1.f / (den + 1e-16f);
-    for (int base = r0; base < r1; base += 64) {
-      const int ne = min(64, r1 - base);
-      if (lane < ne) {
-        const int s = cs[base + lane];
-        sb[wv][lane] = s * 256;
-        wl[wv][lane] = __expf(lrelu(asad[(size_t)s * 2] + adv) - m) * dinv;
-      }
+
+  for (int grp = blockIdx.x; grp < N / 4; grp += gridDim.x) {
+    const int n = grp * 4 + wv;
+    const int r0 = rp[n], r1 = rp[n + 1];
+    const int deg = r1 - r0;
+    const float adv = asad[(size_t)n * 2 + 1];
+    float a0 = 0.f, a1 = 0.f;
+
+    auto fma2 = [&](uint32_t v, float w) { a0 += w * bflo(v); a1 += w * bfhi(v); };
+
+    if (deg <= 64) {
+      const bool valid = lane < deg;
+      int s = 0;
+      float e = -1e30f;
+      if (valid) { s = cs[r0 + lane]; e = lrelu(asad[(size_t)s * 2] + adv); }
+      float m = e;
+#pragma unroll
+      for (int d = 1; d < 64; d <<= 1) m = fmaxf(m, __shfl_xor(m, d));
+      float x = valid ? __expf(e - m) : 0.f;
+      float den = x;
+#pragma unroll
+      for (int d = 1; d < 64; d <<= 1) den += __shfl_xor(den, d);
+      if (valid) { sb[wv * 64 + lane] = s * 256; wl[wv * 64 + lane] = x / (den + 1e-16f); }
       __builtin_amdgcn_wave_barrier();
-      for (int g = 0; g < ne; ++g)
-        fma2(*(const uint32_t*)(fb + (size_t)sb[wv][g] + loff), wl[wv][g]);
-      __builtin_amdgcn_wave_barrier();
-    }
+      int g = 0;
+      for (; g + 8 <= deg; g += 8) {
+        uint32_t b[8];
+        float w[8];
+#pragma unroll
+        for (int k = 0; k < 8; ++k) {
+          b[k] = *(const uint32_t*)(fb + (size_t)sb[wv * 64 + g + k] + loff);
+          w[k] = wl[wv * 64 + g + k];
+        }
+#pragma unroll
+        for (int k = 0; k < 8; ++k) { a0 += w[k] * bflo(b[k]); a1 += w[k] * bfhi(b[k]); }
+      }
+      for (; g < deg; ++g)
+        fma2(*(const uint32_t*)(fb + (size_t)sb[wv * 64 + g] + loff), wl[wv * 64 + g]);
+    } else {
+      float m = -1e30f;
+      for (int i = r0 + lane; i < r1; i += 64) m = fmaxf(m, lrelu(asad[(size_t)cs[i] * 2] + adv));
+#pragma unroll
+      for (int d = 1; d < 64; d <<= 1) m = fmaxf(m, __shfl_xor(m, d));
+      float den = 0.f;
+      for (int i = r0 + lane; i < r1; i += 64) den += __expf(lrelu(asad[(size_t)cs[i] * 2] + adv) - m);
+#pragma unroll
+      for (int d = 1; d < 64; d <<= 1) den += __shfl_xor(den, d);
+      const float dinv = 1.f / (den + 1e-16f);
+      for (int base = r0; base < r1; base += 64) {
+        const int ne = min(64, r1 - base);
+        if (lane < ne) {
+          const int s = cs[base + lane];
+          sb[wv * 64 + lane] = s * 256;
+          wl[wv * 64 + lane] = __expf(lrelu(asad[(size_t)s * 2] + adv) - m) * dinv;
+        }
+        __builtin_amdgcn_wave_barrier();
+        for (int g = 0; g < ne; ++g)
+          fma2(*(const uint32_t*)(fb + (size_t)sb[wv * 64 + g] + loff), wl[wv * 64 + g]);
+        __builtin_amdgcn_wave_barrier();
+      }
+    }
+    *(uint32_t*)&agg[(size_t)n * 128 + lane * 2] = pack2bf(a0, a1);
   }
-  *(uint32_t*)&agg[(size_t)n * 128 + lane * 2] = pack2bf(a0, a1);
-}
-
-
-__global__ __launch_bounds__(256) void mlp_tail(const bf16_t* __restrict__ A,
-                                                const bf16_t* __restrict__ M3t,
-                                                const float* __restrict__ bm,
-                                                const bf16_t* __restrict__ l2t,
-                                                const float* __restrict__ l2b,
-                                                const bf16_t* __restrict__ l3t,
-                                                const float* __restrict__ l3b,
-                                                float* __restrict__ out, int M) {
-  __shared__ __align__(16) bf16_t As[128 * 128];
-  __shared__ __align__(16) bf16_t Ws[128 * 128];
-  const int t = threadIdx.x, wave = t >> 6, lane = t & 63;
-  const int ln15 = lane & 15, quad = lane >> 4;
-  const int bmr = blockIdx.x * 128;
-  const int rowLim = M - 1 - bmr;
-
-#pragma unroll
-  for (int r = 0; r < 8; ++r) {
-    int base = (wave * 8 + r) * 1024;
-    int flat = base + lane * 16;
-    int row = flat >> 8;
-    int grow = row < rowLim ? row : rowLim;
-    const char* gp = (const char*)A + (size_t)grow * 256 + (flat & 255);
-    __builtin_amdgcn_global_load_lds((const AS1 void*)gp,
-                                     (AS3 void*)((char*)As + base), 16, 0, 0);
-  }
-#pragma unroll
-  for (int r = 0; r < 8; ++r) {
-    int base = (wave * 8 + r) * 1024;
-    __builtin_amdgcn_global_load_lds((const AS1 void*)((const char*)M3t + base + lane * 16),
-                                     (AS3 void*)((char*)Ws + base), 16, 0, 0);
-  }
-  __syncthreads();
-
-  const int wm = wave * 32;
-  f32x4 a1[2][8];
-#pragma unroll
-  for (int mi = 0; mi < 2; ++mi)
-#pragma unroll
-    for (int ni = 0; ni < 8; ++ni) a1[mi][ni] = (f32x4){0.f, 0.f, 0.f, 0.f};
-#pragma unroll
-  for (int kk = 0; kk < 128; kk += 32) {
-    bf16x8 af[2];
-#pragma unroll
-    for (int mi = 0; mi < 2; ++mi)
-      af[mi] = *(const bf16x8*)&As[(wm + mi * 16 + ln15) * 128 + kk + quad * 8];
-#pragma unroll
-    for (int ni = 0; ni < 8; ++ni) {
-      bf16x8 bf = *(const bf16x8*)&Ws[(ni * 16 + ln15) * 128 + kk + quad * 8];
-#pragma unroll
-      for (int mi = 0; mi < 2; ++mi)
-        a1[mi][ni] = __builtin_amdgcn_mfma_f32_16x16x32_bf16(af[mi], bf, a1[mi][ni], 0, 0, 0);
-    }
-  }
-  __syncthreads();
-
-#pragma unroll
-  for (int r = 0; r < 4; ++r) {
-    int base = (wave * 4 + r) * 1024;
-    __builtin_amdgcn_global_load_lds((const AS1 void*)((const char*)l2t + base + lane * 16),
-                                     (AS3 void*)((char*)Ws + base), 16, 0, 0);
-  }
-#pragma unroll
-  for (int r = 0; r < 2; ++r) {
-    int base = (wave * 2 + r) * 1024;
-    __builtin_amdgcn_global_load_lds((const AS1 void*)((const char*)l3t + base + lane * 16),
-                                     (AS3 void*)((char*)Ws + 8192 * 2 + base), 16, 0, 0);
-  }
-#pragma unroll
-  for (int mi = 0; mi < 2; ++mi) {
-    int r0 = wm + mi * 16 + quad * 4;
-#pragma unroll
-    for (int ni = 0; ni < 8; ++ni) {
-      int c = ni * 16 + ln15;
-      float bv = bm[c];
-#pragma unroll
-      for (int reg = 0; reg < 4; ++reg)
-        As[(r0 + reg) * 128 + c] = (bf16_t)fmaxf(a1[mi][ni][reg] + bv, 0.f);
-    }
-  }
-  __syncthreads();
-
-  f32x4 a2[2][4];
-#pragma unroll
-  for (int mi = 0; mi < 2; ++mi)
-#pragma unroll
-    for (int ni = 0; ni < 4; ++ni) a2[mi][ni] = (f32x4){0.f, 0.f, 0.f, 0.f};
-#pragma unroll
-  for (int kk = 0; kk < 128; kk += 32) {
-    bf16x8 af[2];
-#pragma unroll
-    for (int mi = 0; mi < 2; ++mi)
-      af[mi] = *(const bf16x8*)&As[(wm + mi * 16 + ln15) * 128 + kk + quad * 8];
-#pragma unroll
-    for (int ni = 0; ni < 4; ++ni) {
-      bf16x8 bf = *(const bf16x8*)&Ws[(ni * 16 + ln15) * 128 + kk + quad * 8];
-#pragma unroll
-      for (int mi = 0; mi < 2; ++mi)
-        a2[mi][ni] = __builtin_amdgcn_mfma_f32_16x16x32_bf16(af[mi], bf, a2[mi][ni], 0, 0, 0);
-    }
-  }
-  __syncthreads();
-
-#pragma unroll
-  for (int mi = 0; mi < 2; ++mi) {
-    int r0 = wm + mi * 16 + quad * 4;
-#pragma unroll
-    for (int ni = 0; ni < 4; ++ni) {
-      int c = ni * 16 + ln15;
-      float bv = l2b[c];
-#pragma unroll
-      for (int reg = 0; reg < 4; ++reg)
-        As[(r0 + reg) * 64 + c] = (bf16_t)fmaxf(a2[mi][ni][reg] + bv, 0.f);
-    }
-  }
-  __syncthreads();
-
-  f32x4 a3[2][4];
-#pragma unroll
-  for (int mi = 0; mi < 2; ++mi)
-#pragma unroll
-    for (int ni = 0; ni < 4; ++ni) a3[mi][ni] = (f32x4){0.f, 0.f, 0.f, 0.f};
-#pragma unroll
-  for (int kk = 0; kk < 64; kk += 32) {
-    bf16x8 af[2];
-#pragma unroll
-    for (int mi = 0; mi < 2; ++mi)
-      af[mi] = *(const bf16x8*)&As[(wm + mi * 16 + ln15) * 64 + kk + quad * 8];
-#pragma unroll
-    for (int ni = 0; ni < 4; ++ni) {
-      bf16x8 bf = *(const bf16x8*)&Ws[8192 + (ni * 16 + ln15) * 64 + kk + quad * 8];
-#pragma unroll
-      for (int mi = 0; mi < 2; ++mi)
-        a3[mi][ni] = __builtin_amdgcn_mfma_f32_16x16x32_bf16(af[mi], bf, a3[mi][ni], 0, 0, 0);
-    }
-  }
-#pragma unroll
-  for (int mi = 0; mi < 2; ++mi) {
-    int r0 = wm + mi * 16 + quad * 4;
-#pragma unroll
-    for (int ni = 0; ni < 4; ++ni) {
-      int c = ni * 16 + ln15;
-      float bv = l3b[c];
-#pragma unroll
-      for (int reg = 0; reg < 4; ++reg) {
-        int r = bmr + r0 + reg;
-        if (r < M) {
-          float v = a3[mi][ni][reg] + bv;
-          out[(size_t)r * 64 + c] = 1.f / (1.f + __expf(-v));
-        }
-      }
-    }
-  }
+}
+
+
+__global__ void __launch_bounds__(256, 5) mega(MegaArgs a) {
+  __shared__ __align__(16) char smem[24 * 1024];
+  cg::grid_group grid = cg::this_grid();
+
+  for (int b = blockIdx.x; b < a.EB + a.N / 4; b += gridDim.x)
+    scatter_cast_dev(a, b);
+  grid.sync();
+
+  gather4_dev<256>(smem, a.xb, a.asadA, a.rp, a.col, a.aggb, a.N);
+  grid.sync();
+
+  gemm_dev(smem, a.aggb, a.Ws1t, a.b1, a.bn1g, a.bn1b, a.bn1m, a.bn1v, 3,
+           a.f1b, nullptr, a.N, 128, 1024);
+  grid.sync();
+
+  alpha_dev<128, 4>(a.f1b, a.P2, a.asadB, a.N);
+  grid.sync();
+
+  gather4_dev<128>(smem, a.f1b, a.asadB, a.rp, a.col, a.aggb, a.N);
+  grid.sync();
+
+  gemm_dev(smem, a.aggb, a.Ws2t, a.b2, a.bn2g, a.bn2b, a.bn2m, a.bn2v, 3,
+           a.f2b, nullptr, a.N, 128, 512);
+  grid.sync();
+
+  alpha_dev<128, 1>(a.f2b, a.P3, a.asadC, a.N);
+  grid.sync();
+
+  gather1_dev(smem, a.f2b, a.asadC, a.rp, a.col, a.aggb, a.N);
+  grid.sync();
+
+  gemm_dev(smem, a.aggb, a.M3t, a.bm, nullptr, nullptr, nullptr, nullptr, 1,
+           a.f1b, nullptr, a.N, 128, 128);
+  grid.sync();
+
+  gemm_dev(smem, a.f1b, a.l2t, a.l2b, nullptr, nullptr, nullptr, nullptr, 1,
+           a.f2b, nullptr, a.N, 64, 128);
+  grid.sync();
+
+  gemm_dev(smem, a.f2b, a.l3t, a.l3b, nullptr, nullptr, nullptr, nullptr, 2,
+           nullptr, a.out, a.N, 64, 64);
 }
 
 
@@ -799,22 +695,27 @@
   prep1<<<780 + EB, 256, 0, stream>>>(pa);
 
   scan_kernel<<<1, 1024, 0, stream>>>(cnt, row_ptr, cursor, N);
-  scatter_cast<<<EB + N / 4, 256, 0, stream>>>(ei, E, N, EB, cursor, col, x, P1, xb, asadA);
-
-  const int gm = (N + 127) / 128;
-  const int ab = N / 4;
-  const int gb = N / 2;
-
-  gat_agg_in4<256><<<gb, 128, 0, stream>>>(xb, asadA, row_ptr, col, aggb);
-  gemm_mfma<64, 3, bf16_t><<<dim3(gm, 2), 256, 0, stream>>>(
-      aggb, Ws1t, b1, bn1g, bn1b, bn1m, bn1v, f1b, N, 128, 1024);
-
-  alpha_gemm<128, 4><<<ab, 256, 0, stream>>>(f1b, P2, asadB);
-  gat_agg_in4<128><<<gb, 128, 0, stream>>>(f1b, asadB, row_ptr, col, aggb);
-  gemm_mfma<64, 3, bf16_t><<<dim3(gm, 2), 256, 0, stream>>>(
-      aggb, Ws2t, b2, bn2g, bn2b, bn2m, bn2v, f2b, N, 128, 512);
-
-  alpha_gemm<128, 1><<<ab, 256, 0, stream>>>(f2b, P3, asadC);
-  gat_agg_in1<<<gb, 128, 0, stream>>>(f2b, asadC, row_ptr, col, aggb);
-  mlp_tail<<<gm, 256, 0, stream>>>(aggb, M3t, bm, l2t, l2b, l3t, l3b, out, N);
-}
+
+  int maxB = 0;
+  hipOccupancyMaxActiveBlocksPerMultiprocessor(&maxB, mega, 256, 0);
+  if (maxB < 1) maxB = 1;
+  if (maxB > 6) maxB = 6;
+  const int nblk = maxB * 256;
+
+  MegaArgs ma;
+  ma.ei = ei; ma.E = E; ma.N = N; ma.EB = EB;
+  ma.cursor = cursor; ma.col = col;
+  ma.x = x; ma.P1 = P1; ma.xb = xb; ma.asadA = asadA;
+  ma.aggb = aggb; ma.f1b = f1b; ma.f2b = f2b;
+  ma.asadB = asadB; ma.asadC = asadC;
+  ma.rp = row_ptr;
+  ma.Ws1t = Ws1t; ma.Ws2t = Ws2t; ma.M3t = M3t; ma.l2t = l2t; ma.l3t = l3t;
+  ma.P2 = P2; ma.P3 = P3;
+  ma.b1 = b1; ma.bn1g = bn1g; ma.bn1b = bn1b; ma.bn1m = bn1m; ma.bn1v = bn1v;
+  ma.b2 = b2; ma.bn2g = bn2g; ma.bn2b = bn2b; ma.bn2m = bn2m; ma.bn2v = bn2v;
+  ma.bm = bm; ma.l2b = l2b; ma.l3b = l3b;
+  ma.out = out;
+
+  void* kargs[] = {&ma};
+  hipLaunchCooperativeKernel((const void*)mega, dim3(nblk), dim3(256), kargs, 0, stream);
+}
```

After: 1.044 ms. 3.09x slower.
